# Kernel optimization log

Measured on AMD Instinct MI355X. Metric: run time of the kernel, lower is better.

Reference implementation:

```python
import jax, jax.numpy as jnp
import numpy as np
from jax import lax

VSZ, EMB, HID = 32000, 256, 512
B, S, T = 32, 64, 64


def _lstm_scan(xs, h0, c0, Wih, Whh, b):
    # xs: [L, B, D_in]; returns all hidden states [L, B, H], final (h, c)
    def step(carry, x):
        h, c = carry
        g = x @ Wih.T + h @ Whh.T + b  # [B, 4H]
        i, f, gg, o = jnp.split(g, 4, axis=-1)
        c = jax.nn.sigmoid(f) * c + jax.nn.sigmoid(i) * jnp.tanh(gg)
        h = jax.nn.sigmoid(o) * jnp.tanh(c)
        return (h, c), h
    (h, c), hs = lax.scan(step, (h0, c0), xs)
    return hs, h, c


def setup_inputs() -> dict:
    key = jax.random.key(0)
    ks = jax.random.split(key, 24)
    sc = 0.02
    d = {}
    d['src'] = jax.random.randint(ks[0], (B, S), 0, VSZ)
    d['tgt'] = jax.random.randint(ks[1], (B, T), 0, VSZ)
    enc_emb = jax.random.normal(ks[2], (VSZ, EMB), jnp.float32) * sc
    d['enc_emb'] = enc_emb.at[0].set(0.0)  # padding_idx=0
    dec_emb = jax.random.normal(ks[3], (VSZ, EMB), jnp.float32) * sc
    d['dec_emb'] = dec_emb.at[0].set(0.0)
    # encoder bidirectional LSTM (fwd / bwd directions)
    d['Wih_f'] = jax.random.normal(ks[4], (4 * HID, EMB), jnp.float32) * sc
    d['Whh_f'] = jax.random.normal(ks[5], (4 * HID, HID), jnp.float32) * sc
    d['b_f'] = jnp.zeros((4 * HID,), jnp.float32)
    d['Wih_b'] = jax.random.normal(ks[6], (4 * HID, EMB), jnp.float32) * sc
    d['Whh_b'] = jax.random.normal(ks[7], (4 * HID, HID), jnp.float32) * sc
    d['b_b'] = jnp.zeros((4 * HID,), jnp.float32)
    # enc_proj: Linear(2H -> H)
    d['encW'] = jax.random.normal(ks[8], (HID, 2 * HID), jnp.float32) * sc
    d['encb'] = jnp.zeros((HID,), jnp.float32)
    # decoder LSTM: input EMB + HID
    d['dWih'] = jax.random.normal(ks[9], (4 * HID, EMB + HID), jnp.float32) * sc
    d['dWhh'] = jax.random.normal(ks[10], (4 * HID, HID), jnp.float32) * sc
    d['db'] = jnp.zeros((4 * HID,), jnp.float32)
    # attn: Linear(2H -> 1)
    d['attnW'] = jax.random.normal(ks[11], (1, 2 * HID), jnp.float32) * sc
    d['attnb'] = jnp.zeros((1,), jnp.float32)
    # proj: Linear(H -> V)
    d['projW'] = jax.random.normal(ks[12], (VSZ, HID), jnp.float32) * sc
    d['projb'] = jnp.zeros((VSZ,), jnp.float32)
    return d


def reference(src, tgt, enc_emb, dec_emb, Wih_f, Whh_f, b_f, Wih_b, Whh_b, b_b,
              encW, encb, dWih, dWhh, db, attnW, attnb, projW, projb):
    # ---- encoder ----
    emb = enc_emb[src]                       # [B, S, E]
    xs = jnp.transpose(emb, (1, 0, 2))       # [S, B, E]
    h0 = jnp.zeros((B, HID), emb.dtype)
    hs_f, hT_f, _ = _lstm_scan(xs, h0, h0, Wih_f, Whh_f, b_f)
    hs_b, hT_b, _ = _lstm_scan(xs[::-1], h0, h0, Wih_b, Whh_b, b_b)
    hs_b = hs_b[::-1]
    enc_cat = jnp.concatenate([hs_f, hs_b], axis=-1)        # [S, B, 2H]
    enc_out = jnp.transpose(enc_cat, (1, 0, 2)) @ encW.T + encb  # [B, S, H]
    h = jnp.tanh(jnp.concatenate([hT_f, hT_b], axis=-1) @ encW.T + encb)  # [B, H]
    c = jnp.zeros_like(h)

    # split attn weight: scores = attn([dec_h, enc_out]) = dec_h@w1 + enc_out@w2 + b
    w1, w2 = attnW[:, :HID], attnW[:, HID:]
    enc_score = enc_out @ w2.T               # [B, S, 1] precomputed

    # ---- decoder (teacher forcing, tf = 1.0 for determinism) ----
    def dec_step(carry, tok):
        h, c = carry
        e = dec_emb[tok]                     # [B, E]
        scores = (h @ w1.T)[:, None, :] + enc_score + attnb   # [B, S, 1]
        w = jax.nn.softmax(scores, axis=1)
        ctx = jnp.sum(w * enc_out, axis=1)   # [B, H]
        x = jnp.concatenate([e, ctx], axis=-1)
        g = x @ dWih.T + h @ dWhh.T + db
        i, f, gg, o = jnp.split(g, 4, axis=-1)
        c = jax.nn.sigmoid(f) * c + jax.nn.sigmoid(i) * jnp.tanh(gg)
        h = jax.nn.sigmoid(o) * jnp.tanh(c)
        logits = h @ projW.T + projb         # [B, V]
        return (h, c), logits

    toks = tgt[:, :-1].T                     # [T-1, B] input token per step
    _, logits = lax.scan(dec_step, (h, c), toks)   # [T-1, B, V]
    outs = jnp.concatenate(
        [jnp.zeros((B, 1, VSZ), logits.dtype), jnp.transpose(logits, (1, 0, 2))],
        axis=1)                              # [B, T, V]; step 0 left as zeros
    return outs
```

## Files before the change

kernel.cpp:

```cpp
#include <hip/hip_runtime.h>
#include <math.h>

#define B_ 32
#define S_ 64
#define T_ 64
#define EMB_ 256
#define HID_ 512
#define VSZ_ 32000
#define G4_ 2048

#define O_XWF    0
#define O_XWB    4194304
#define O_HSCAT  8388608
#define O_ENCOUT 10485760
#define O_CTX    11534336
#define O_HDEC   11550720
#define O_CBUF   12599296
#define O_WTF    12648448
#define O_WTB    13697024
#define O_WTD    14745600

__global__ __launch_bounds__(256) void k_transpose(
    const float* __restrict__ Wf, const float* __restrict__ Wb,
    const float* __restrict__ Wd,
    float* __restrict__ Of, float* __restrict__ Ob, float* __restrict__ Od)
{
    __shared__ float ld[32][33];
    const int z = blockIdx.z;
    const float* W = (z == 0) ? Wf : (z == 1) ? Wb : Wd;
    float* O = (z == 0) ? Of : (z == 1) ? Ob : Od;
    const int t = threadIdx.x;
    const int jt = blockIdx.x * 32, kt = blockIdx.y * 32;
    {
        int kl = t & 31, jl4 = t >> 5;
        #pragma unroll
        for (int jj = 0; jj < 4; ++jj) {
            int j = jl4 + jj * 8;
            ld[j][kl] = W[(size_t)(jt + j) * 512 + kt + kl];
        }
    }
    __syncthreads();
    {
        int jl = t & 31, kg = t >> 5;
        int j = jt + jl;
        int jp = ((j & 511) << 2) | (j >> 9);
        #pragma unroll
        for (int ii = 0; ii < 4; ++ii) {
            int k = kg * 4 + ii;
            O[(size_t)(kt + k) * 2048 + jp] = ld[jl][k];
        }
    }
}

template<int MODE, int K>
__global__ __launch_bounds__(256) void k_gemm(
    const float* __restrict__ A0, const float* __restrict__ A1,
    const int*   __restrict__ I0,
    const float* __restrict__ W0, const float* __restrict__ W1,
    const float* __restrict__ bias0, const float* __restrict__ bias1,
    float* __restrict__ C0, float* __restrict__ C1, float* __restrict__ C2,
    int M)
{
    __shared__ float As[16][132];
    __shared__ float Bs[16][132];

    const int t = threadIdx.x;
    const int m0 = blockIdx.y * 128;
    const int n0 = blockIdx.x * 128;
    const int z = blockIdx.z;
    const int tm8 = (t >> 4) * 8;
    const int tn8 = (t & 15) * 8;

    const float* W    = (MODE == 0 && z == 1) ? W1 : W0;
    const float* Bp   = (MODE == 0 && z == 1) ? bias1 : bias0;
    float*       Cout = (MODE == 0 && z == 1) ? C1 : C0;

    auto loadA = [&](int r, int k) -> float4 {
        if constexpr (MODE == 0) {
            int s = r >> 5, b = r & 31;
            int id = I0[b * 64 + s];
            return *(const float4*)&A0[(size_t)id * 256 + k];
        } else if constexpr (MODE == 1) {
            if (r < 2048) {
                int b = r >> 6, s = r & 63;
                return *(const float4*)&A0[s * 32768 + b * 1024 + k];
            } else {
                int b = r - 2048;
                return *(const float4*)&A0[(k < 512 ? 63 * 32768 : 0) + b * 1024 + k];
            }
        } else if constexpr (MODE == 2) {
            int tt = r >> 5, b = r & 31;
            if (k < 256) {
                int id = I0[b * 64 + tt];
                return *(const float4*)&A0[(size_t)id * 256 + k];
            } else {
                return *(const float4*)&A1[b * 512 + (k - 256)];
            }
        } else {
            return *(const float4*)&A0[(size_t)r * 512 + k];
        }
    };

    float acc[8][8];
    #pragma unroll
    for (int i = 0; i < 8; ++i)
        #pragma unroll
        for (int j = 0; j < 8; ++j) acc[i][j] = 0.f;

    for (int k0 = 0; k0 < K; k0 += 16) {
        #pragma unroll
        for (int i2 = 0; i2 < 2; ++i2) {
            int slot = t + i2 * 256;
            int rl = slot >> 2, kq = slot & 3;
            int kk0 = k0 + kq * 4;
            float4 av = make_float4(0.f, 0.f, 0.f, 0.f);
            if (m0 + rl < M) av = loadA(m0 + rl, kk0);
            As[kq * 4 + 0][rl] = av.x; As[kq * 4 + 1][rl] = av.y;
            As[kq * 4 + 2][rl] = av.z; As[kq * 4 + 3][rl] = av.w;
            float4 bv = *(const float4*)&W[(size_t)(n0 + rl) * K + kk0];
            Bs[kq * 4 + 0][rl] = bv.x; Bs[kq * 4 + 1][rl] = bv.y;
            Bs[kq * 4 + 2][rl] = bv.z; Bs[kq * 4 + 3][rl] = bv.w;
        }
        __syncthreads();
        #pragma unroll
        for (int kk = 0; kk < 16; ++kk) {
            float a[8], b[8];
            *(float4*)&a[0] = *(const float4*)&As[kk][tm8];
            *(float4*)&a[4] = *(const float4*)&As[kk][tm8 + 4];
            *(float4*)&b[0] = *(const float4*)&Bs[kk][tn8];
            *(float4*)&b[4] = *(const float4*)&Bs[kk][tn8 + 4];
            #pragma unroll
            for (int i = 0; i < 8; ++i)
                #pragma unroll
                for (int j = 0; j < 8; ++j)
                    acc[i][j] = fmaf(a[i], b[j], acc[i][j]);
        }
        __syncthreads();
    }

    #pragma unroll
    for (int i = 0; i < 8; ++i) {
        int r = m0 + tm8 + i;
        if (r >= M) break;
        #pragma unroll
        for (int j = 0; j < 8; ++j) {
            int n = n0 + tn8 + j;
            float v = acc[i][j] + Bp[n];
            if constexpr (MODE == 0) {
                int s = r >> 5, b = r & 31;
                int np = ((n & 511) << 2) | (n >> 9);
                Cout[s * 65536 + b * 2048 + np] = v;
            } else if constexpr (MODE == 1) {
                if (r < 2048) Cout[r * 512 + n] = v;
                else          C2[(r - 2048) * 512 + n] = tanhf(v);
            } else if constexpr (MODE == 2) {
                int tt = r >> 5, b = r & 31;
                int np = ((n & 511) << 2) | (n >> 9);
                Cout[tt * 65536 + b * 2048 + np] = v;
            } else {
                int tt = r >> 5, b = r & 31;
                Cout[(size_t)b * 2048000 + (size_t)(tt + 1) * 32000 + n] = v;
            }
        }
    }
}

__global__ __launch_bounds__(256) void k_gates(
    int mode, int i,
    const float* __restrict__ xwf, const float* __restrict__ xwb,
    const float* __restrict__ wtf, const float* __restrict__ wtb,
    float* __restrict__ hscat, float* __restrict__ hdec0,
    float* __restrict__ cbase)
{
    __shared__ float hT[512][8];
    __shared__ float red[8][8][32][4];

    const int t = threadIdx.x;
    const int bid = blockIdx.x;

    int dir, cgT, bT, zero_h, zero_c, hstr;
    const float *xw, *wt, *hsrc;
    float *hdst, *cb;
    if (mode == 0) {
        const int xcd = bid & 7;
        dir = xcd >> 2;
        const int idx = ((bid >> 3) << 2) + (xcd & 3);
        cgT = idx & 15; bT = idx >> 4;
        const int s = dir ? (63 - i) : i;
        xw = (dir ? xwb : xwf) + s * 65536;
        wt = dir ? wtb : wtf;
        const int sp = dir ? (s + 1) : (s - 1);
        hsrc = hscat + sp * 32768 + dir * 512;
        hdst = hscat + s  * 32768 + dir * 512;
        hstr = 1024;
        cb = cbase + dir * 16384;
        zero_h = (i == 0); zero_c = (i == 0);
    } else {
        cgT = bid & 15; bT = bid >> 4;
        dir = 0;
        xw = xwf + i * 65536;
        wt = wtf;
        hsrc = hdec0 + (i - 1) * 16384;
        hdst = hdec0 + i * 16384;
        hstr = 512;
        cb = cbase + 32768;
        zero_h = 0; zero_c = (i == 0);
    }
    const int b0  = bT * 8;
    const int cg0 = cgT * 32;

    if (!zero_h) {
        const int bb = t & 7, kq = t >> 3;
        #pragma unroll
        for (int j = 0; j < 4; ++j) {
            const int k = kq * 16 + j * 4;
            const float4 h4 = *(const float4*)&hsrc[(b0 + bb) * hstr + k];
            hT[k + 0][bb] = h4.x; hT[k + 1][bb] = h4.y;
            hT[k + 2][bb] = h4.z; hT[k + 3][bb] = h4.w;
        }
    }
    __syncthreads();

    const int cgl = t & 31, kh = t >> 5;
    const int cg = cg0 + cgl;

    float4 acc[8];
    #pragma unroll
    for (int b = 0; b < 8; ++b) acc[b] = make_float4(0.f, 0.f, 0.f, 0.f);

    if (!zero_h) {
        const float4* wt4 = (const float4*)wt;
        #pragma unroll 4
        for (int j = 0; j < 64; ++j) {
            const int k = j * 8 + kh;
            const float4 w = wt4[(size_t)k * 512 + cg];
            float hv[8];
            *(float4*)&hv[0] = *(const float4*)&hT[k][0];
            *(float4*)&hv[4] = *(const float4*)&hT[k][4];
            #pragma unroll
            for (int b = 0; b < 8; ++b) {
                acc[b].x = fmaf(hv[b], w.x, acc[b].x);
                acc[b].y = fmaf(hv[b], w.y, acc[b].y);
                acc[b].z = fmaf(hv[b], w.z, acc[b].z);
                acc[b].w = fmaf(hv[b], w.w, acc[b].w);
            }
        }
        #pragma unroll
        for (int b = 0; b < 8; ++b)
            *(float4*)&red[kh][b][cgl][0] = acc[b];
    }
    __syncthreads();

    const int cgl2 = t & 31, bb2 = t >> 5;
    const int b_g = b0 + bb2, cg_g = cg0 + cgl2;

    float4 g = *(const float4*)&xw[b_g * 2048 + cg_g * 4];
    if (!zero_h) {
        #pragma unroll
        for (int kh2 = 0; kh2 < 8; ++kh2) {
            const float4 p = *(const float4*)&red[kh2][bb2][cgl2][0];
            g.x += p.x; g.y += p.y; g.z += p.z; g.w += p.w;
        }
    }
    const float iv = 1.f / (1.f + expf(-g.x));
    const float fv = 1.f / (1.f + expf(-g.y));
    const float gv = tanhf(g.z);
    const float ov = 1.f / (1.f + expf(-g.w));
    const float cold = zero_c ? 0.f : cb[b_g * 512 + cg_g];
    const float cn = fv * cold + iv * gv;
    cb[b_g * 512 + cg_g] = cn;
    hdst[b_g * hstr + cg_g] = ov * tanhf(cn);
}

__global__ __launch_bounds__(256) void k_ctx(
    const float* __restrict__ encout, const float* __restrict__ attnW,
    float* __restrict__ ctx)
{
    __shared__ float red[256];
    __shared__ float sc[64];
    const int b = blockIdx.x;
    const int t = threadIdx.x;
    const float* eb = encout + b * 64 * 512;
    const float* w2 = attnW + 512;

    int s = t >> 2, part = t & 3;
    float p = 0.f;
    for (int h = part * 128; h < part * 128 + 128; ++h)
        p += eb[s * 512 + h] * w2[h];
    red[t] = p;
    __syncthreads();
    if (part == 0) sc[s] = red[t] + red[t + 1] + red[t + 2] + red[t + 3];
    __syncthreads();
    if (t == 0) {
        float mx = -1e30f;
        for (int s2 = 0; s2 < 64; ++s2) mx = fmaxf(mx, sc[s2]);
        float sum = 0.f;
        for (int s2 = 0; s2 < 64; ++s2) { sc[s2] = expf(sc[s2] - mx); sum += sc[s2]; }
        float inv = 1.f / sum;
        for (int s2 = 0; s2 < 64; ++s2) sc[s2] *= inv;
    }
    __syncthreads();
    for (int h = t; h < 512; h += 256) {
        float a = 0.f;
        for (int s2 = 0; s2 < 64; ++s2) a += sc[s2] * eb[s2 * 512 + h];
        ctx[b * 512 + h] = a;
    }
}

__global__ __launch_bounds__(256) void k_zero0(float* __restrict__ out)
{
    int idx = blockIdx.x * 256 + threadIdx.x;
    int b = idx / 8000, v = idx % 8000;
    ((float4*)out)[(size_t)b * 512000 + v] = make_float4(0.f, 0.f, 0.f, 0.f);
}

extern "C" void kernel_launch(void* const* d_in, const int* in_sizes, int n_in,
                              void* d_out, int out_size, void* d_ws, size_t ws_size,
                              hipStream_t stream)
{
    const int*   src     = (const int*)  d_in[0];
    const int*   tgt     = (const int*)  d_in[1];
    const float* enc_emb = (const float*)d_in[2];
    const float* dec_emb = (const float*)d_in[3];
    const float* Wih_f   = (const float*)d_in[4];
    const float* Whh_f   = (const float*)d_in[5];
    const float* b_f     = (const float*)d_in[6];
    const float* Wih_b   = (const float*)d_in[7];
    const float* Whh_b   = (const float*)d_in[8];
    const float* b_b     = (const float*)d_in[9];
    const float* encW    = (const float*)d_in[10];
    const float* encb    = (const float*)d_in[11];
    const float* dWih    = (const float*)d_in[12];
    const float* dWhh    = (const float*)d_in[13];
    const float* db      = (const float*)d_in[14];
    const float* attnW   = (const float*)d_in[15];
    const float* projW   = (const float*)d_in[17];
    const float* projb   = (const float*)d_in[18];
    float* out = (float*)d_out;
    float* ws  = (float*)d_ws;

    float* xw_f    = ws + O_XWF;
    float* xw_b    = ws + O_XWB;
    float* hscat   = ws + O_HSCAT;
    float* encout  = ws + O_ENCOUT;
    float* ctx     = ws + O_CTX;
    float* hdec_m1 = ws + O_HDEC;
    float* hdec0   = hdec_m1 + 16384;
    float* cb      = ws + O_CBUF;
    float* wtf     = ws + O_WTF;
    float* wtb     = ws + O_WTB;
    float* wtd     = ws + O_WTD;
    float* pre     = xw_f;

    k_transpose<<<dim3(64, 16, 3), 256, 0, stream>>>(Whh_f, Whh_b, dWhh, wtf, wtb, wtd);

    k_gemm<0, 256><<<dim3(16, 16, 2), 256, 0, stream>>>(
        enc_emb, nullptr, src, Wih_f, Wih_b, b_f, b_b, xw_f, xw_b, nullptr, 2048);

    for (int i = 0; i < 64; ++i)
        k_gates<<<dim3(128), 256, 0, stream>>>(
            0, i, xw_f, xw_b, wtf, wtb, hscat, nullptr, cb);

    k_gemm<1, 1024><<<dim3(4, 17, 1), 256, 0, stream>>>(
        hscat, nullptr, nullptr, encW, nullptr, encb, nullptr,
        encout, nullptr, hdec_m1, 2080);

    k_ctx<<<dim3(32), 256, 0, stream>>>(encout, attnW, ctx);

    k_gemm<2, 768><<<dim3(16, 16, 1), 256, 0, stream>>>(
        dec_emb, ctx, tgt, dWih, nullptr, db, nullptr, pre, nullptr, nullptr, 2016);

    for (int t = 0; t < 63; ++t)
        k_gates<<<dim3(64), 256, 0, stream>>>(
            1, t, pre, nullptr, wtd, nullptr, nullptr, hdec0, cb);

    k_zero0<<<dim3(1000), 256, 0, stream>>>(out);
    k_gemm<3, 512><<<dim3(250, 16, 1), 256, 0, stream>>>(
        hdec0, nullptr, nullptr, projW, nullptr, projb, nullptr,
        out, nullptr, nullptr, 2016);
}
```

Before: 2.520 ms.

## Run vocab projection GEMM on bf16 MFMA with split hi/lo precision

```diff
diff --git a/kernel.cpp b/kernel.cpp
--- a/kernel.cpp
+++ b/kernel.cpp
@@ -8,6 +8,9 @@
 #define HID_ 512
 #define VSZ_ 32000
 #define G4_ 2048
+
+typedef __attribute__((ext_vector_type(8))) short short8;
+typedef __attribute__((ext_vector_type(4))) float f32x4;
 
 #define O_XWF    0
 #define O_XWB    4194304
@@ -19,6 +22,15 @@
 #define O_WTF    12648448
 #define O_WTB    13697024
 #define O_WTD    14745600
+
+__device__ __forceinline__ unsigned short f2bf(float x) {
+    unsigned int u = __float_as_uint(x);
+    u = (u + 0x7fffu + ((u >> 16) & 1u)) >> 16;
+    return (unsigned short)u;
+}
+__device__ __forceinline__ float bf2f(unsigned short h) {
+    return __uint_as_float(((unsigned int)h) << 16);
+}
 
 __global__ __launch_bounds__(256) void k_transpose(
     const float* __restrict__ Wf, const float* __restrict__ Wb,
@@ -88,7 +100,7 @@
                 int b = r - 2048;
                 return *(const float4*)&A0[(k < 512 ? 63 * 32768 : 0) + b * 1024 + k];
             }
-        } else if constexpr (MODE == 2) {
+        } else {
             int tt = r >> 5, b = r & 31;
             if (k < 256) {
                 int id = I0[b * 64 + tt];
@@ -96,8 +108,6 @@
             } else {
                 return *(const float4*)&A1[b * 512 + (k - 256)];
             }
-        } else {
-            return *(const float4*)&A0[(size_t)r * 512 + k];
         }
     };
 
@@ -153,13 +163,10 @@
             } else if constexpr (MODE == 1) {
                 if (r < 2048) Cout[r * 512 + n] = v;
                 else          C2[(r - 2048) * 512 + n] = tanhf(v);
-            } else if constexpr (MODE == 2) {
+            } else {
                 int tt = r >> 5, b = r & 31;
                 int np = ((n & 511) << 2) | (n >> 9);
                 Cout[tt * 65536 + b * 2048 + np] = v;
-            } else {
-                int tt = r >> 5, b = r & 31;
-                Cout[(size_t)b * 2048000 + (size_t)(tt + 1) * 32000 + n] = v;
             }
         }
     }
@@ -314,6 +321,118 @@
     ((float4*)out)[(size_t)b * 512000 + v] = make_float4(0.f, 0.f, 0.f, 0.f);
 }
 
+__global__ __launch_bounds__(256) void k_cvt(
+    const float* __restrict__ X, unsigned short* __restrict__ hi,
+    unsigned short* __restrict__ lo, int n4)
+{
+    int i = blockIdx.x * 256 + threadIdx.x;
+    if (i >= n4) return;
+    float4 v = ((const float4*)X)[i];
+    ushort4 h, l;
+    h.x = f2bf(v.x); l.x = f2bf(v.x - bf2f(h.x));
+    h.y = f2bf(v.y); l.y = f2bf(v.y - bf2f(h.y));
+    h.z = f2bf(v.z); l.z = f2bf(v.z - bf2f(h.z));
+    h.w = f2bf(v.w); l.w = f2bf(v.w - bf2f(h.w));
+    ((ushort4*)hi)[i] = h;
+    ((ushort4*)lo)[i] = l;
+}
+
+__global__ __launch_bounds__(256, 2) void k_vmfma(
+    const unsigned short* __restrict__ Ahi, const unsigned short* __restrict__ Alo,
+    const unsigned short* __restrict__ Whi, const unsigned short* __restrict__ Wlo,
+    const float* __restrict__ bias, float* __restrict__ out, int n_base)
+{
+    __shared__ unsigned short Ah[128 * 64], Al[128 * 64];
+    __shared__ unsigned short Bh[128 * 64], Bl[128 * 64];
+
+    const int t  = threadIdx.x;
+    const int m0 = blockIdx.y * 128;
+    const int n0 = blockIdx.x * 128;
+    const int l  = t & 63, w = t >> 6;
+    const int wm = w >> 1, wn = w & 1;
+
+    const int jj = t & 7;
+    const int rl = t >> 3;
+
+    f32x4 acc[4][4];
+    #pragma unroll
+    for (int mi = 0; mi < 4; ++mi)
+        #pragma unroll
+        for (int ni = 0; ni < 4; ++ni)
+            acc[mi][ni] = (f32x4)0.f;
+
+    const short8 zero8 = (short8)0;
+
+    for (int kt = 0; kt < 8; ++kt) {
+        const int k0 = kt * 64;
+        #pragma unroll
+        for (int i = 0; i < 4; ++i) {
+            const int row  = rl + 32 * i;
+            const int lane = (jj & 3) * 16 + (row & 15);
+            const int slot = ((row >> 4) * 2 + (jj >> 2)) * 64 + lane;
+            const size_t goff = (size_t)k0 + jj * 8;
+
+            const int am = m0 + row;
+            short8 va = zero8, vb = zero8;
+            if (am < 2016) {
+                va = *(const short8*)&Ahi[(size_t)am * 512 + goff];
+                vb = *(const short8*)&Alo[(size_t)am * 512 + goff];
+            }
+            *(short8*)&Ah[slot * 8] = va;
+            *(short8*)&Al[slot * 8] = vb;
+
+            const int bn = n0 + row;
+            *(short8*)&Bh[slot * 8] = *(const short8*)&Whi[(size_t)bn * 512 + goff];
+            *(short8*)&Bl[slot * 8] = *(const short8*)&Wlo[(size_t)bn * 512 + goff];
+        }
+        __syncthreads();
+
+        #pragma unroll
+        for (int s = 0; s < 2; ++s) {
+            short8 ah[4], al[4];
+            #pragma unroll
+            for (int mi = 0; mi < 4; ++mi) {
+                const int slot = ((wm * 4 + mi) * 2 + s) * 64 + l;
+                ah[mi] = *(const short8*)&Ah[slot * 8];
+                al[mi] = *(const short8*)&Al[slot * 8];
+            }
+            #pragma unroll
+            for (int ni = 0; ni < 4; ++ni) {
+                const int slot = ((wn * 4 + ni) * 2 + s) * 64 + l;
+                const short8 bh = *(const short8*)&Bh[slot * 8];
+                const short8 bl = *(const short8*)&Bl[slot * 8];
+                #pragma unroll
+                for (int mi = 0; mi < 4; ++mi) {
+                    acc[mi][ni] = __builtin_amdgcn_mfma_f32_16x16x32_bf16(ah[mi], bh, acc[mi][ni], 0, 0, 0);
+                    acc[mi][ni] = __builtin_amdgcn_mfma_f32_16x16x32_bf16(ah[mi], bl, acc[mi][ni], 0, 0, 0);
+                    acc[mi][ni] = __builtin_amdgcn_mfma_f32_16x16x32_bf16(al[mi], bh, acc[mi][ni], 0, 0, 0);
+                }
+            }
+        }
+        __syncthreads();
+    }
+
+    #pragma unroll
+    for (int ni = 0; ni < 4; ++ni) {
+        const int n = n0 + wn * 64 + ni * 16 + (l & 15);
+        const int v = n_base + n;
+        const float bv = bias[v];
+        #pragma unroll
+        for (int mi = 0; mi < 4; ++mi) {
+            const int mbase = m0 + wm * 64 + mi * 16 + ((l >> 4) << 2);
+            #pragma unroll
+            for (int r = 0; r < 4; ++r) {
+                const int m = mbase + r;
+                if (m < 2016) {
+                    const int tt = m >> 5, b = m & 31;
+                    out[(size_t)b * 2048000 + (size_t)(tt + 1) * 32000 + v] =
+                        acc[mi][ni][r] + bv;
+                }
+            }
+        }
+    }
+}
+
 extern "C" void kernel_launch(void* const* d_in, const int* in_sizes, int n_in,
                               void* d_out, int out_size, void* d_ws, size_t ws_size,
                               hipStream_t stream)
@@ -352,6 +471,11 @@
     float* wtd     = ws + O_WTD;
     float* pre     = xw_f;
 
+    unsigned short* Whi = (unsigned short*)(ws + O_XWF);
+    unsigned short* Wlo = (unsigned short*)(ws + O_XWB);
+    unsigned short* Ahi = (unsigned short*)(ws + O_HSCAT);
+    unsigned short* Alo = (unsigned short*)(ws + O_HSCAT + 524288);
+
     k_transpose<<<dim3(64, 16, 3), 256, 0, stream>>>(Whh_f, Whh_b, dWhh, wtf, wtb, wtd);
 
     k_gemm<0, 256><<<dim3(16, 16, 2), 256, 0, stream>>>(
@@ -375,7 +499,11 @@
             1, t, pre, nullptr, wtd, nullptr, nullptr, hdec0, cb);
 
     k_zero0<<<dim3(1000), 256, 0, stream>>>(out);
-    k_gemm<3, 512><<<dim3(250, 16, 1), 256, 0, stream>>>(
-        hdec0, nullptr, nullptr, projW, nullptr, projb, nullptr,
-        out, nullptr, nullptr, 2016);
-}
+    k_cvt<<<dim3(1008), 256, 0, stream>>>(hdec0, Ahi, Alo, 258048);
+    for (int c = 0; c < 2; ++c) {
+        k_cvt<<<dim3(8000), 256, 0, stream>>>(
+            projW + (size_t)c * 16000 * 512, Whi, Wlo, 2048000);
+        k_vmfma<<<dim3(125, 16), 256, 0, stream>>>(
+            Ahi, Alo, Whi, Wlo, projb, out, c * 16000);
+    }
+}
```

Result: faster. 2.103 ms (-16.5%).
